# Optimization experiments

Hardware: AMD Instinct MI355X
Metric: run time of the kernel (lower is better)

Reference implementation:

```python
import jax, jax.numpy as jnp
import numpy as np

B, E, N, H, F = 16, 8192, 384, 32, 16


def _forward(edge_feat, node_feat, edge_index, edge_mask, num_ligand_atoms,
             structural_w, plip_protein_w, plip_ligand_w, plip_inter_w,
             loc_w, virtual_w, W1, b1, W2, b2):
    n_graph, max_e, _ = edge_feat.shape
    n_node = node_feat.shape[1]
    codes = edge_feat[:, :, :3].astype(jnp.int32)          # [B,E,3] edge type codes
    dist = edge_feat[:, :, 3:4]                            # [B,E,1]
    c0, c1, c2 = codes[..., 0], codes[..., 1], codes[..., 2]
    src = edge_index[:, 0, :]                              # [B,E]
    tgt = edge_index[:, 1, :]
    nl = num_ligand_atoms[:, None]
    src_lig = src < nl
    tgt_lig = tgt < nl

    # structural edges: c0 in {0,1} -> idx = c0*4 + c1*2 + c2
    struct_idx = jnp.clip(c0 * 4 + c1 * 2 + c2, 0, 19)
    struct_emb = structural_w[struct_idx]                  # [B,E,H]

    # PLIP edges: c0 == 5 -> table chosen by ligand membership + location emb
    pi = jnp.clip(c1, 0, 14)
    both_lig = src_lig & tgt_lig
    both_prot = (~src_lig) & (~tgt_lig)
    plip_emb = jnp.where(both_lig[..., None], plip_ligand_w[pi],
                         jnp.where(both_prot[..., None], plip_protein_w[pi], plip_inter_w[pi]))
    loc = jnp.where(both_lig, 0, jnp.where(both_prot, 1, 2))
    plip_emb = plip_emb + loc_w[loc]

    is_struct = (c0 == 0) | (c0 == 1)
    is_plip = c0 == 5
    type_emb = jnp.where(is_struct[..., None], struct_emb,
                         jnp.where(is_plip[..., None], plip_emb, 0.0))

    # distance MLP: Linear(1,H) -> ReLU -> Linear(H,H)
    h = jax.nn.relu(dist @ W1.T + b1)                      # [B,E,H]
    dist_emb = h @ W2.T + b2

    keep = edge_mask & ~((src == 0) & (tgt == 0))
    edge_emb = jnp.where(keep[..., None], type_emb + dist_emb, 0.0)  # [B,E,H]

    # scatter-add into bias [B, N+1, N+1, H] (symmetric), offset +1 for graph token
    s1 = src + 1
    t1 = tgt + 1
    valid = edge_mask & (src >= 0) & (src < n_node) & (tgt >= 0) & (tgt < n_node)
    s_idx = jnp.where(valid, s1, 0)
    t_idx = jnp.where(valid, t1, 0)
    val = jnp.where(valid[..., None], edge_emb, 0.0)
    b_idx = jnp.broadcast_to(jnp.arange(n_graph)[:, None], (n_graph, max_e))

    bias = jnp.zeros((n_graph, n_node + 1, n_node + 1, H), dtype=edge_feat.dtype)
    bias = bias.at[b_idx, s_idx, t_idx].add(val)
    bias = bias.at[b_idx, t_idx, s_idx].add(val)

    # graph-token virtual distance
    t = virtual_w[0]                                       # [H]
    bias = bias.at[:, 1:, 0, :].add(t)
    bias = bias.at[:, 0, :, :].add(t)
    return jnp.transpose(bias, (0, 3, 1, 2))               # [B,H,N+1,N+1]


def setup_inputs() -> dict:
    key = jax.random.key(0)
    ks = jax.random.split(key, 16)
    c0 = jax.random.randint(ks[0], (B, E), 0, 7)
    c1 = jnp.where(c0 <= 1, jax.random.randint(ks[1], (B, E), 0, 2),
                   jax.random.randint(ks[2], (B, E), 0, 15))
    c2 = jax.random.randint(ks[3], (B, E), 0, 2)
    dist = jax.random.uniform(ks[4], (B, E, 1)) * 10.0
    edge_feat = jnp.concatenate([jnp.stack([c0, c1, c2], -1).astype(jnp.float32), dist], -1)
    edge_index = jax.random.randint(ks[5], (B, 2, E), 0, N).astype(jnp.int32)
    edge_mask = jax.random.uniform(ks[6], (B, E)) > 0.1
    num_ligand_atoms = jax.random.randint(ks[7], (B,), 1, N).astype(jnp.int32)
    node_feat = jax.random.normal(ks[8], (B, N, F), dtype=jnp.float32)
    std_e = 0.02
    std_l = 0.02 / np.sqrt(12.0)
    structural_w = (jax.random.normal(ks[9], (20, H)) * std_e).at[0].set(0.0)
    plip_protein_w = (jax.random.normal(ks[10], (15, H)) * std_e).at[0].set(0.0)
    plip_ligand_w = (jax.random.normal(ks[11], (15, H)) * std_e).at[0].set(0.0)
    plip_inter_w = (jax.random.normal(ks[12], (15, H)) * std_e).at[0].set(0.0)
    loc_w = jax.random.normal(ks[13], (4, H)) * std_e
    virtual_w = jax.random.normal(ks[14], (1, H)) * std_e
    W1 = jax.random.normal(ks[15], (H, 1)) * std_l
    W2 = jax.random.normal(jax.random.fold_in(key, 99), (H, H)) * std_l
    b1 = jnp.zeros((H,), jnp.float32)
    b2 = jnp.zeros((H,), jnp.float32)
    return dict(edge_feat=edge_feat, node_feat=node_feat, edge_index=edge_index,
                edge_mask=edge_mask, num_ligand_atoms=num_ligand_atoms,
                structural_w=structural_w, plip_protein_w=plip_protein_w,
                plip_ligand_w=plip_ligand_w, plip_inter_w=plip_inter_w,
                loc_w=loc_w, virtual_w=virtual_w, W1=W1, b1=b1, W2=W2, b2=b2)


def reference(edge_feat, node_feat, edge_index, edge_mask, num_ligand_atoms,
              structural_w, plip_protein_w, plip_ligand_w, plip_inter_w,
              loc_w, virtual_w, W1, b1, W2, b2):
    return _forward(edge_feat, node_feat, edge_index, edge_mask, num_ligand_atoms,
                    structural_w, plip_protein_w, plip_ligand_w, plip_inter_w,
                    loc_w, virtual_w, W1, b1, W2, b2)
```

## Files before the change

### kernel.cpp

```cpp
#include <hip/hip_runtime.h>
#include <hip/hip_bf16.h>

#define B_  16
#define E_  8192
#define NN_ 384
#define N1_ 385
#define H_  32
#define HH_ 16
#define PLANE_ (N1_ * N1_)
#define TOTAL_ (B_ * H_ * PLANE_)
#define CAP_ 128
#define NBIN_ (B_ * N1_)
#define STRIDE_ 396
#define TS_ 20
#define CHUNK_ 5
#define NCH_ 77

#define WS_COUNTS 0
#define WS_T      32768
#define WS_A      33024
#define WS_B      (33024 + 33*32*4)
#define WS_BINS2  65536
#define WS_NEED   ((size_t)WS_BINS2 + (size_t)NBIN_*CAP_*8)


__global__ __launch_bounds__(256) void prep_kernel(
    const float* __restrict__ W1, const float* __restrict__ b1,
    const float* __restrict__ W2, const float* __restrict__ b2,
    float* __restrict__ T, float* __restrict__ A, float* __restrict__ Bv,
    int* __restrict__ counts)
{
    int g = blockIdx.x * 256 + threadIdx.x;
    if (g < NBIN_) counts[g] = 0;

    if (blockIdx.x == 0) {
        __shared__ float sTv[32], sT[32], sW1[32], sb1[32];
        int tid = threadIdx.x;
        if (tid < 32) {
            float w = W1[tid], b = b1[tid];
            sW1[tid] = w; sb1[tid] = b;
            sTv[tid] = (w != 0.0f) ? (-b / w) : -3.402823e38f;
        }
        __syncthreads();
        if (tid < 32) {
            float t = sTv[tid];
            int rank = 0;
            for (int j = 0; j < 32; ++j) {
                float tj = sTv[j];
                rank += (tj < t || (tj == t && j < tid)) ? 1 : 0;
            }
            sT[rank] = t;
        }
        __syncthreads();
        if (tid < 32) T[tid] = sT[tid];
        for (int idx = tid; idx < 33 * 32; idx += 256) {
            int s = idx >> 5, h = idx & 31;
            float m;
            if (s == 0)       m = sT[0] - 1.0f;
            else if (s == 32) m = sT[31] + 1.0f;
            else              m = 0.5f * (sT[s - 1] + sT[s]);
            float alpha = b2[h], beta = 0.0f;
            for (int k = 0; k < 32; ++k) {
                float w = sW1[k], b = sb1[k];
                bool act = (w > 0.0f) ? (m > -b / w)
                         : (w < 0.0f) ? (m < -b / w) : (b > 0.0f);
                if (act) {
                    float w2 = W2[h * 32 + k];
                    alpha = fmaf(w2, b, alpha);
                    beta  = fmaf(w2, w, beta);
                }
            }
            A[idx] = alpha; Bv[idx] = beta;
        }
    }
}

__global__ __launch_bounds__(256) void bin_kernel(
    const float4* __restrict__ edge_feat,
    const int*    __restrict__ edge_index,
    const void*   __restrict__ edge_mask,
    const int*    __restrict__ nlig,
    int* __restrict__ counts, int2* __restrict__ bins2)
{
    int lane = threadIdx.x & 63;
    int probe = ((const int*)edge_mask)[lane];
    bool byte_mask = __any(probe != 0 && probe != 1);

    int gid = blockIdx.x * blockDim.x + threadIdx.x;
    int b = gid >> 13, e = gid & (E_ - 1);
    bool m = byte_mask ? (((const unsigned char*)edge_mask)[gid] != 0)
                       : (((const int*)edge_mask)[gid] != 0);
    if (!m) return;
    int src = edge_index[(b * 2 + 0) * E_ + e];
    int tgt = edge_index[(b * 2 + 1) * E_ + e];
    if (src < 0 || src >= NN_ || tgt < 0 || tgt >= NN_) return;
    if (src == 0 && tgt == 0) return;

    float4 ef = edge_feat[gid];
    int c0 = (int)ef.x, c1 = (int)ef.y, c2 = (int)ef.z;
    float dist = ef.w;

    int r;
    if (c0 == 0 || c0 == 1) {
        r = min(max(c0 * 4 + c1 * 2 + c2, 0), 19);
    } else if (c0 == 5) {
        int pi = min(max(c1, 0), 14);
        int nl = nlig[b];
        bool sl = src < nl, tl = tgt < nl;
        int loc = (sl && tl) ? 0 : ((!sl && !tl) ? 1 : 2);
        r = 20 + loc * 15 + pi;
    } else r = 65;

    int s1 = src + 1, t1 = tgt + 1;
    int db = __float_as_int(dist);
    int bin1 = b * N1_ + s1, bin2 = b * N1_ + t1;
    int p = atomicAdd(&counts[bin1], 1);
    if (p < CAP_) bins2[bin1 * CAP_ + p] = make_int2((r << 9) | t1, db);
    p = atomicAdd(&counts[bin2], 1);
    if (p < CAP_) bins2[bin2 * CAP_ + p] = make_int2((r << 9) | s1, db);
}

__global__ __launch_bounds__(256, 4) void chunk_kernel(
    const float* __restrict__ structural_w,
    const float* __restrict__ plip_protein_w,
    const float* __restrict__ plip_ligand_w,
    const float* __restrict__ plip_inter_w,
    const float* __restrict__ loc_w,
    const float* __restrict__ virtual_w,
    const float* __restrict__ T,
    const float* __restrict__ A,
    const float* __restrict__ Bv,
    const int*   __restrict__ counts,
    const int2*  __restrict__ bins2,
    float* __restrict__ out)
{
    __shared__ float srow[HH_ * STRIDE_];
    __shared__ float sA[33 * TS_], sB[33 * TS_];
    __shared__ float sType[66 * TS_];

    int bid = blockIdx.x;
    int chunk = bid % NCH_;
    int rest  = bid / NCH_;
    int half = rest & 1;
    int b = rest >> 1;
    int h0 = half << 4;
    int tid = threadIdx.x;
    int wv = tid >> 6, lane = tid & 63;

    for (int idx = tid; idx < 33 * 16; idx += 256) {
        int s = idx >> 4, hh = idx & 15;
        sA[s * TS_ + hh] = A[s * 32 + h0 + hh];
        sB[s * TS_ + hh] = Bv[s * 32 + h0 + hh];
    }
    for (int idx = tid; idx < 66 * 16; idx += 256) {
        int r = idx >> 4, hh = idx & 15;
        float v;
        if (r < 20) v = structural_w[r * 32 + h0 + hh];
        else if (r < 65) {
            int t2 = r - 20;
            int loc = t2 / 15, pi = t2 - loc * 15;
            const float* pw = (loc == 0) ? plip_ligand_w
                            : (loc == 1) ? plip_protein_w : plip_inter_w;
            v = pw[pi * 32 + h0 + hh] + loc_w[loc * 32 + h0 + hh];
        } else v = 0.0f;
        sType[r * TS_ + hh] = v;
    }

    float tr[32];
#pragma unroll
    for (int q = 0; q < 8; ++q) {
        float4 tv = *reinterpret_cast<const float4*>(T + 4 * q);
        tr[4 * q] = tv.x; tr[4 * q + 1] = tv.y; tr[4 * q + 2] = tv.z; tr[4 * q + 3] = tv.w;
    }
    __syncthreads();

    int hh_q = lane & 3;
    int slot = lane >> 2;
    int hhg  = (wv << 2) | hh_q;
    int hq   = h0 + hhg;
    float* sW = srow + (wv << 2) * STRIDE_;

    int rw = lane >> 4;
    int sl = lane & 15;
    int hw = h0 + (wv << 2) + rw;

    int i0 = chunk * CHUNK_;
#pragma unroll 1
    for (int ii = 0; ii < CHUNK_; ++ii) {
        int i = i0 + ii;
        int rowid = b * N1_ + i;

#pragma unroll
        for (int r = 0; r < 4; ++r) {
            float vw = virtual_w[h0 + (wv << 2) + r];
            float fill = (i == 0) ? vw : 0.0f;
            float4 f4 = make_float4(fill, fill, fill, fill);
            float4* rp = reinterpret_cast<float4*>(sW + r * STRIDE_);
            for (int c = lane; c < STRIDE_ / 4; c += 64) rp[c] = f4;
        }
        if (i != 0 && lane < 4) {
            int hr = h0 + (wv << 2) + lane;
            int off = (4 - ((hr + i) & 3)) & 3;
            sW[lane * STRIDE_ + 4 - off] = virtual_w[hr];
        }

        int cnt = counts[rowid]; cnt = cnt < CAP_ ? cnt : CAP_;
        int offq = (4 - ((hq + i) & 3)) & 3;
        int base = hh_q * STRIDE_ + 4 - offq;
        for (int j = slot; j < cnt; j += 16) {
            int2 e2 = bins2[rowid * CAP_ + j];
            float dist = __int_as_float(e2.y);
            int other = e2.x & 0x1FF;
            int r = e2.x >> 9;
            int lo = 0;
#pragma unroll
            for (int k = 0; k < 32; ++k) lo += (tr[k] < dist) ? 1 : 0;
            float acc = fmaf(dist, sB[lo * TS_ + hhg], sA[lo * TS_ + hhg])
                      + sType[r * TS_ + hhg];
            atomicAdd(&sW[base + other], acc);
        }

        {
            const float* rr = sW + rw * STRIDE_;
            float* dst = out + ((size_t)(b * H_ + hw)) * PLANE_ + (size_t)i * N1_;
            int off = (4 - ((hw + i) & 3)) & 3;
            if (sl < off) dst[sl] = rr[4 - off + sl];
            int nvec = (N1_ - off) >> 2;
            for (int q = sl; q < nvec; q += 16) {
                float4 v = *reinterpret_cast<const float4*>(rr + 4 + 4 * q);
                *reinterpret_cast<float4*>(dst + off + 4 * q) = v;
            }
            int done = off + (nvec << 2);
            int rem = N1_ - done;
            if (sl < rem) dst[done + sl] = rr[4 + 4 * nvec + sl];
        }
    }
}


__global__ __launch_bounds__(256) void init_out_kernel(
    float* __restrict__ out, const float* __restrict__ virtual_w)
{
    unsigned int tid = blockIdx.x * blockDim.x + threadIdx.x;
    unsigned int base = tid * 4u;
    if (base >= (unsigned int)TOTAL_) return;
    float4 v; float* pv = &v.x;
#pragma unroll
    for (int u = 0; u < 4; ++u) {
        unsigned int idx = base + u;
        unsigned int bh     = idx / (unsigned int)PLANE_;
        unsigned int within = idx - bh * (unsigned int)PLANE_;
        unsigned int h = bh & (H_ - 1);
        unsigned int i = within / (unsigned int)N1_;
        unsigned int j = within - i * (unsigned int)N1_;
        pv[u] = (i == 0u || j == 0u) ? virtual_w[h] : 0.0f;
    }
    *reinterpret_cast<float4*>(out + base) = v;
}

__global__ __launch_bounds__(256) void edge_kernel(
    const float4* __restrict__ edge_feat, const int* __restrict__ edge_index,
    const void* __restrict__ edge_mask, const int* __restrict__ nlig,
    const float* __restrict__ structural_w, const float* __restrict__ plip_protein_w,
    const float* __restrict__ plip_ligand_w, const float* __restrict__ plip_inter_w,
    const float* __restrict__ loc_w, const float* __restrict__ W1,
    const float* __restrict__ b1, const float* __restrict__ W2,
    const float* __restrict__ b2, float* __restrict__ out)
{
    __shared__ float sW2[H_ * H_];
    __shared__ float sW1[H_], sb1[H_], sb2[H_];
    __shared__ float sStruct[20 * H_];
    __shared__ float sPlipP[15 * H_], sPlipL[15 * H_], sPlipI[15 * H_];
    __shared__ float sLoc[4 * H_];

    for (int i = threadIdx.x; i < H_ * H_; i += blockDim.x) sW2[i] = W2[i];
    if (threadIdx.x < H_) {
        sW1[threadIdx.x] = W1[threadIdx.x];
        sb1[threadIdx.x] = b1[threadIdx.x];
        sb2[threadIdx.x] = b2[threadIdx.x];
    }
    for (int i = threadIdx.x; i < 20 * H_; i += blockDim.x) sStruct[i] = structural_w[i];
    for (int i = threadIdx.x; i < 15 * H_; i += blockDim.x) {
        sPlipP[i] = plip_protein_w[i]; sPlipL[i] = plip_ligand_w[i]; sPlipI[i] = plip_inter_w[i];
    }
    for (int i = threadIdx.x; i < 4 * H_; i += blockDim.x) sLoc[i] = loc_w[i];

    int lane = threadIdx.x & 63;
    int probe = ((const int*)edge_mask)[lane];
    bool byte_mask = __any(probe != 0 && probe != 1);
    __syncthreads();

    int gid = blockIdx.x * blockDim.x + threadIdx.x;
    int b = gid >> 13, e = gid & (E_ - 1);
    bool m = byte_mask ? (((const unsigned char*)edge_mask)[gid] != 0)
                       : (((const int*)edge_mask)[gid] != 0);
    if (!m) return;
    int src = edge_index[(b * 2 + 0) * E_ + e];
    int tgt = edge_index[(b * 2 + 1) * E_ + e];
    if (src < 0 || src >= NN_ || tgt < 0 || tgt >= NN_) return;
    if (src == 0 && tgt == 0) return;

    float4 ef = edge_feat[gid];
    int c0 = (int)ef.x, c1 = (int)ef.y, c2 = (int)ef.z;
    float dist = ef.w;
    const float* type_ptr = nullptr; const float* loc_ptr = nullptr;
    if (c0 == 0 || c0 == 1) {
        int si = min(max(c0 * 4 + c1 * 2 + c2, 0), 19);
        type_ptr = &sStruct[si * H_];
    } else if (c0 == 5) {
        int pi = min(max(c1, 0), 14);
        int nl = nlig[b];
        bool sl = src < nl, tl = tgt < nl;
        const float* pw; int loc;
        if (sl && tl)        { pw = sPlipL; loc = 0; }
        else if (!sl && !tl) { pw = sPlipP; loc = 1; }
        else                 { pw = sPlipI; loc = 2; }
        type_ptr = &pw[pi * H_]; loc_ptr = &sLoc[loc * H_];
    }
    float hk[H_];
#pragma unroll
    for (int k = 0; k < H_; ++k) {
        float v = fmaf(dist, sW1[k], sb1[k]);
        hk[k] = v > 0.0f ? v : 0.0f;
    }
    int s1 = src + 1, t1 = tgt + 1;
    float* outb = out + (size_t)b * H_ * PLANE_;
    int off1 = s1 * N1_ + t1, off2 = t1 * N1_ + s1;
#pragma unroll 4
    for (int h = 0; h < H_; ++h) {
        float acc = sb2[h];
#pragma unroll
        for (int k = 0; k < H_; ++k) acc = fmaf(hk[k], sW2[h * H_ + k], acc);
        if (type_ptr) acc += type_ptr[h];
        if (loc_ptr)  acc += loc_ptr[h];
        float* p = outb + (size_t)h * PLANE_;
        unsafeAtomicAdd(p + off1, acc);
        unsafeAtomicAdd(p + off2, acc);
    }
}

extern "C" void kernel_launch(void* const* d_in, const int* in_sizes, int n_in,
                              void* d_out, int out_size, void* d_ws, size_t ws_size,
                              hipStream_t stream)
{
    const float4* edge_feat      = (const float4*)d_in[0];
    const int*    edge_index     = (const int*)  d_in[2];
    const void*   edge_mask      =               d_in[3];
    const int*    nlig           = (const int*)  d_in[4];
    const float*  structural_w   = (const float*)d_in[5];
    const float*  plip_protein_w = (const float*)d_in[6];
    const float*  plip_ligand_w  = (const float*)d_in[7];
    const float*  plip_inter_w   = (const float*)d_in[8];
    const float*  loc_w          = (const float*)d_in[9];
    const float*  virtual_w      = (const float*)d_in[10];
    const float*  W1             = (const float*)d_in[11];
    const float*  b1             = (const float*)d_in[12];
    const float*  W2             = (const float*)d_in[13];
    const float*  b2             = (const float*)d_in[14];
    float* out = (float*)d_out;

    if (ws_size >= WS_NEED) {
        char* ws = (char*)d_ws;
        int*   counts = (int*)  (ws + WS_COUNTS);
        float* T      = (float*)(ws + WS_T);
        float* A      = (float*)(ws + WS_A);
        float* Bv     = (float*)(ws + WS_B);
        int2*  bins2  = (int2*) (ws + WS_BINS2);

        prep_kernel<<<25, 256, 0, stream>>>(W1, b1, W2, b2, T, A, Bv, counts);
        bin_kernel<<<(B_ * E_) / 256, 256, 0, stream>>>(
            edge_feat, edge_index, edge_mask, nlig, counts, bins2);
        chunk_kernel<<<B_ * 2 * NCH_, 256, 0, stream>>>(
            structural_w, plip_protein_w, plip_ligand_w, plip_inter_w,
            loc_w, virtual_w, T, A, Bv, counts, bins2, out);
    } else {
        unsigned int nth  = (unsigned int)(TOTAL_ / 4);
        unsigned int nblk = (nth + 255u) / 256u;
        init_out_kernel<<<nblk, 256, 0, stream>>>(out, virtual_w);
        edge_kernel<<<(B_ * E_) / 256, 256, 0, stream>>>(
            edge_feat, edge_index, edge_mask, nlig,
            structural_w, plip_protein_w, plip_ligand_w, plip_inter_w,
            loc_w, W1, b1, W2, b2, out);
    }
}
```

Before: 117.5 us.

## Precompute distance segment index in bin kernel and widen chunk blocks to 512 threads

New measurement: 96.14 us. 18.2% less time.

```diff
diff --git a/kernel.cpp b/kernel.cpp
--- a/kernel.cpp
+++ b/kernel.cpp
@@ -12,7 +12,7 @@
 #define CAP_ 128
 #define NBIN_ (B_ * N1_)
 #define STRIDE_ 396
-#define TS_ 20
+#define TS_ 21
 #define CHUNK_ 5
 #define NCH_ 77
 
@@ -80,6 +80,7 @@
     const int*    __restrict__ edge_index,
     const void*   __restrict__ edge_mask,
     const int*    __restrict__ nlig,
+    const float*  __restrict__ T,
     int* __restrict__ counts, int2* __restrict__ bins2)
 {
     int lane = threadIdx.x & 63;
@@ -111,32 +112,43 @@
         r = 20 + loc * 15 + pi;
     } else r = 65;
 
+    int lo = 0;
+#pragma unroll
+    for (int q = 0; q < 8; ++q) {
+        float4 tv = *reinterpret_cast<const float4*>(T + 4 * q);
+        lo += (tv.x < dist) ? 1 : 0;
+        lo += (tv.y < dist) ? 1 : 0;
+        lo += (tv.z < dist) ? 1 : 0;
+        lo += (tv.w < dist) ? 1 : 0;
+    }
+
     int s1 = src + 1, t1 = tgt + 1;
     int db = __float_as_int(dist);
-    int bin1 = b * N1_ + s1, bin2 = b * N1_ + t1;
+    int base = (lo << 16) | (r << 9);
+    int bin1 = b * N1_ + s1, bin2i = b * N1_ + t1;
     int p = atomicAdd(&counts[bin1], 1);
-    if (p < CAP_) bins2[bin1 * CAP_ + p] = make_int2((r << 9) | t1, db);
-    p = atomicAdd(&counts[bin2], 1);
-    if (p < CAP_) bins2[bin2 * CAP_ + p] = make_int2((r << 9) | s1, db);
-}
-
-__global__ __launch_bounds__(256, 4) void chunk_kernel(
+    if (p < CAP_) bins2[bin1 * CAP_ + p] = make_int2(base | t1, db);
+    p = atomicAdd(&counts[bin2i], 1);
+    if (p < CAP_) bins2[bin2i * CAP_ + p] = make_int2(base | s1, db);
+}
+
+__global__ __launch_bounds__(512, 8) void chunk_kernel(
     const float* __restrict__ structural_w,
     const float* __restrict__ plip_protein_w,
     const float* __restrict__ plip_ligand_w,
     const float* __restrict__ plip_inter_w,
     const float* __restrict__ loc_w,
     const float* __restrict__ virtual_w,
-    const float* __restrict__ T,
     const float* __restrict__ A,
     const float* __restrict__ Bv,
     const int*   __restrict__ counts,
     const int2*  __restrict__ bins2,
     float* __restrict__ out)
 {
-    __shared__ float srow[HH_ * STRIDE_];
+    __shared__ float4 srow4[HH_ * (STRIDE_ / 4)];
     __shared__ float sA[33 * TS_], sB[33 * TS_];
     __shared__ float sType[66 * TS_];
+    float* srow = reinterpret_cast<float*>(srow4);
 
     int bid = blockIdx.x;
     int chunk = bid % NCH_;
@@ -147,12 +159,19 @@
     int tid = threadIdx.x;
     int wv = tid >> 6, lane = tid & 63;
 
-    for (int idx = tid; idx < 33 * 16; idx += 256) {
+    int i0 = chunk * CHUNK_;
+    int rowid0 = b * N1_ + i0;
+
+    int cnts[CHUNK_];
+#pragma unroll
+    for (int ii = 0; ii < CHUNK_; ++ii) cnts[ii] = counts[rowid0 + ii];
+
+    for (int idx = tid; idx < 33 * 16; idx += 512) {
         int s = idx >> 4, hh = idx & 15;
         sA[s * TS_ + hh] = A[s * 32 + h0 + hh];
         sB[s * TS_ + hh] = Bv[s * 32 + h0 + hh];
     }
-    for (int idx = tid; idx < 66 * 16; idx += 256) {
+    for (int idx = tid; idx < 66 * 16; idx += 512) {
         int r = idx >> 4, hh = idx & 15;
         float v;
         if (r < 20) v = structural_w[r * 32 + h0 + hh];
@@ -166,55 +185,48 @@
         sType[r * TS_ + hh] = v;
     }
 
-    float tr[32];
-#pragma unroll
-    for (int q = 0; q < 8; ++q) {
-        float4 tv = *reinterpret_cast<const float4*>(T + 4 * q);
-        tr[4 * q] = tv.x; tr[4 * q + 1] = tv.y; tr[4 * q + 2] = tv.z; tr[4 * q + 3] = tv.w;
-    }
+    int hh_q = lane & 1;
+    int slot = lane >> 1;
+    int hhg  = (wv << 1) | hh_q;
+    int hq   = h0 + hhg;
+    float* sW = srow + (wv << 1) * STRIDE_;
+
+    int rw = lane >> 5;
+    int sl = lane & 31;
+    int hw = h0 + (wv << 1) + rw;
+    float vw0 = virtual_w[h0 + (wv << 1)];
+    float vw1 = virtual_w[h0 + (wv << 1) + 1];
+
     __syncthreads();
 
-    int hh_q = lane & 3;
-    int slot = lane >> 2;
-    int hhg  = (wv << 2) | hh_q;
-    int hq   = h0 + hhg;
-    float* sW = srow + (wv << 2) * STRIDE_;
-
-    int rw = lane >> 4;
-    int sl = lane & 15;
-    int hw = h0 + (wv << 2) + rw;
-
-    int i0 = chunk * CHUNK_;
 #pragma unroll 1
     for (int ii = 0; ii < CHUNK_; ++ii) {
         int i = i0 + ii;
-        int rowid = b * N1_ + i;
-
-#pragma unroll
-        for (int r = 0; r < 4; ++r) {
-            float vw = virtual_w[h0 + (wv << 2) + r];
-            float fill = (i == 0) ? vw : 0.0f;
+        int rowid = rowid0 + ii;
+
+#pragma unroll
+        for (int r = 0; r < 2; ++r) {
+            float vwr = (r == 0) ? vw0 : vw1;
+            float fill = (i == 0) ? vwr : 0.0f;
             float4 f4 = make_float4(fill, fill, fill, fill);
             float4* rp = reinterpret_cast<float4*>(sW + r * STRIDE_);
             for (int c = lane; c < STRIDE_ / 4; c += 64) rp[c] = f4;
         }
-        if (i != 0 && lane < 4) {
-            int hr = h0 + (wv << 2) + lane;
+        if (i != 0 && lane < 2) {
+            int hr = h0 + (wv << 1) + lane;
             int off = (4 - ((hr + i) & 3)) & 3;
-            sW[lane * STRIDE_ + 4 - off] = virtual_w[hr];
-        }
-
-        int cnt = counts[rowid]; cnt = cnt < CAP_ ? cnt : CAP_;
+            sW[lane * STRIDE_ + 4 - off] = (lane == 0) ? vw0 : vw1;
+        }
+
+        int cnt = cnts[ii]; cnt = cnt < CAP_ ? cnt : CAP_;
         int offq = (4 - ((hq + i) & 3)) & 3;
         int base = hh_q * STRIDE_ + 4 - offq;
-        for (int j = slot; j < cnt; j += 16) {
+        for (int j = slot; j < cnt; j += 32) {
             int2 e2 = bins2[rowid * CAP_ + j];
             float dist = __int_as_float(e2.y);
             int other = e2.x & 0x1FF;
-            int r = e2.x >> 9;
-            int lo = 0;
-#pragma unroll
-            for (int k = 0; k < 32; ++k) lo += (tr[k] < dist) ? 1 : 0;
+            int r     = (e2.x >> 9) & 0x7F;
+            int lo    = e2.x >> 16;
             float acc = fmaf(dist, sB[lo * TS_ + hhg], sA[lo * TS_ + hhg])
                       + sType[r * TS_ + hhg];
             atomicAdd(&sW[base + other], acc);
@@ -226,7 +238,7 @@
             int off = (4 - ((hw + i) & 3)) & 3;
             if (sl < off) dst[sl] = rr[4 - off + sl];
             int nvec = (N1_ - off) >> 2;
-            for (int q = sl; q < nvec; q += 16) {
+            for (int q = sl; q < nvec; q += 32) {
                 float4 v = *reinterpret_cast<const float4*>(rr + 4 + 4 * q);
                 *reinterpret_cast<float4*>(dst + off + 4 * q) = v;
             }
@@ -369,10 +381,10 @@
 
         prep_kernel<<<25, 256, 0, stream>>>(W1, b1, W2, b2, T, A, Bv, counts);
         bin_kernel<<<(B_ * E_) / 256, 256, 0, stream>>>(
-            edge_feat, edge_index, edge_mask, nlig, counts, bins2);
-        chunk_kernel<<<B_ * 2 * NCH_, 256, 0, stream>>>(
+            edge_feat, edge_index, edge_mask, nlig, T, counts, bins2);
+        chunk_kernel<<<B_ * 2 * NCH_, 512, 0, stream>>>(
             structural_w, plip_protein_w, plip_ligand_w, plip_inter_w,
-            loc_w, virtual_w, T, A, Bv, counts, bins2, out);
+            loc_w, virtual_w, A, Bv, counts, bins2, out);
     } else {
         unsigned int nth  = (unsigned int)(TOTAL_ / 4);
         unsigned int nblk = (nth + 255u) / 256u;
```
